# Optimization experiments

Hardware: AMD Instinct MI355X
Metric: run time of the kernel (lower is better)

Reference implementation:

```python
import jax, jax.numpy as jnp
import numpy as np

CHUNK = 64
NORM_EPS = 1e-5
DENOM_EPS = 1.0
B, S, HID, H = 4, 4096, 1024, 8
D = HID // H  # 128


def rmsnorm(x, w, eps=NORM_EPS):
    var = jnp.mean(x * x, axis=-1, keepdims=True)
    return x * jax.lax.rsqrt(var + eps) * w


def chunked_linear_attn(q, k, v):
    # q,k,v: [B,S,H,D]; causal linear attention o_s = q_s @ sum_{t<=s} k_t^T v_t
    b, s, h, d = q.shape
    n = s // CHUNK
    def to_chunks(x):
        return x.reshape(b, n, CHUNK, h, d).transpose(1, 0, 3, 2, 4)  # [N,B,H,C,D]
    qc, kc, vc = to_chunks(q), to_chunks(k), to_chunks(v)
    mask = jnp.tril(jnp.ones((CHUNK, CHUNK), dtype=q.dtype))
    def step(state, inp):
        qq, kk, vv = inp  # [B,H,C,D]
        inter = jnp.einsum('bhcd,bhde->bhce', qq, state)
        scores = jnp.einsum('bhcd,bhed->bhce', qq, kk) * mask  # causal intra-chunk
        intra = jnp.einsum('bhce,bhed->bhcd', scores, vv)
        state = state + jnp.einsum('bhcd,bhce->bhde', kk, vv)
        return state, inter + intra
    init = jnp.zeros((b, h, d, d), dtype=q.dtype)
    _, o = jax.lax.scan(step, init, (qc, kc, vc))  # [N,B,H,C,D]
    return o.transpose(1, 0, 3, 2, 4).reshape(b, s, h, d)


def setup_inputs() -> dict:
    key = jax.random.key(0)
    k0, k1, k2, k3, k4 = jax.random.split(key, 5)
    hidden_states = jax.random.normal(k0, (B, S, HID), dtype=jnp.float32)
    Wq = jax.random.normal(k1, (HID, HID), dtype=jnp.float32) * 0.02
    Wk = jax.random.normal(k2, (HID, HID), dtype=jnp.float32) * 0.02
    Wv = jax.random.normal(k3, (HID, HID), dtype=jnp.float32) * 0.02
    Wo = jax.random.normal(k4, (HID, HID), dtype=jnp.float32) * 0.02
    norm_w = jnp.ones((D,), dtype=jnp.float32)
    return {"hidden_states": hidden_states, "Wq": Wq, "Wk": Wk, "Wv": Wv, "Wo": Wo, "norm_w": norm_w}


def reference(hidden_states, Wq, Wk, Wv, Wo, norm_w):
    b, s, _ = hidden_states.shape
    q = jnp.einsum('bsd,ed->bse', hidden_states, Wq).reshape(b, s, H, D)
    k = jnp.einsum('bsd,ed->bse', hidden_states, Wk).reshape(b, s, H, D)
    v = jnp.einsum('bsd,ed->bse', hidden_states, Wv).reshape(b, s, H, D)
    # feature_map='identity', norm_q/norm_k=False
    o = chunked_linear_attn(q, k, v)  # [B,S,H,D]
    z = jnp.cumsum(k, axis=1)
    denom = jnp.maximum(jnp.abs(jnp.sum(q * z, axis=-1)), DENOM_EPS)[..., None]
    o = o / denom
    o = rmsnorm(o, norm_w)
    o = o.reshape(b, s, H * D)
    return jnp.einsum('bse,de->bsd', o, Wo)
```

## Files before the change

kernel.cpp:

```cpp
#include <hip/hip_runtime.h>
#include <stdint.h>

typedef __bf16 bf16x8 __attribute__((ext_vector_type(8)));
typedef float  f32x4  __attribute__((ext_vector_type(4)));

static __device__ __forceinline__ void gload16(const void* g, void* l) {
  __builtin_amdgcn_global_load_lds((__attribute__((address_space(1))) void*)g,
                                   (__attribute__((address_space(3))) void*)l,
                                   16, 0, 0);
}

static __device__ __forceinline__ f32x4 mfma16(bf16x8 a, bf16x8 b, f32x4 c) {
  return __builtin_amdgcn_mfma_f32_16x16x32_bf16(a, b, c, 0, 0, 0);
}

#define MEMFENCE asm volatile("" ::: "memory")

__global__ __launch_bounds__(256) void cast8_k(const float* __restrict__ in,
                                               __bf16* __restrict__ out) {
  const size_t i = ((size_t)blockIdx.x * 256 + threadIdx.x) * 8;
  const float4 v0 = *(const float4*)(in + i);
  const float4 v1 = *(const float4*)(in + i + 4);
  bf16x8 o;
  o[0] = (__bf16)v0.x; o[1] = (__bf16)v0.y; o[2] = (__bf16)v0.z; o[3] = (__bf16)v0.w;
  o[4] = (__bf16)v1.x; o[5] = (__bf16)v1.y; o[6] = (__bf16)v1.z; o[7] = (__bf16)v1.w;
  *(bf16x8*)(out + i) = o;
}

__global__ __launch_bounds__(256) void castw_k(const float* __restrict__ w0, const float* __restrict__ w1,
                                               const float* __restrict__ w2, const float* __restrict__ w3,
                                               __bf16* __restrict__ o0, __bf16* __restrict__ o1,
                                               __bf16* __restrict__ o2, __bf16* __restrict__ o3) {
  const float* in; __bf16* out;
  switch (blockIdx.y) {
    case 0: in = w0; out = o0; break;
    case 1: in = w1; out = o1; break;
    case 2: in = w2; out = o2; break;
    default: in = w3; out = o3; break;
  }
  const size_t i = ((size_t)blockIdx.x * 256 + threadIdx.x) * 8;
  const float4 v0 = *(const float4*)(in + i);
  const float4 v1 = *(const float4*)(in + i + 4);
  bf16x8 o;
  o[0] = (__bf16)v0.x; o[1] = (__bf16)v0.y; o[2] = (__bf16)v0.z; o[3] = (__bf16)v0.w;
  o[4] = (__bf16)v1.x; o[5] = (__bf16)v1.y; o[6] = (__bf16)v1.z; o[7] = (__bf16)v1.w;
  *(bf16x8*)(out + i) = o;
}

static __device__ __forceinline__ void kloop256(
    const __bf16* __restrict__ A, const __bf16* __restrict__ W,
    int m0, int n0, __bf16* sh, int tid, f32x4 acc[8][4]) {
  const int l = tid & 63;
  const int wv = tid >> 6;
  const int wm = wv >> 2, wn = wv & 3;
  const int lo = l & 15, kq = l >> 4;

  auto SA = [&](int kt, int h) {
#pragma unroll
    for (int j = 0; j < 2; ++j) {
      const int p = j * 512 + tid;
      const int r = p >> 3, sl = p & 7;
      const int grow = m0 + h * 64 + (r & 63) + (r >> 6) * 128;
      gload16(A + (size_t)grow * 1024 + (kt << 6) + ((sl ^ (r & 7)) << 3),
              sh + (kt & 1) * 32768 + h * 8192 + p * 8);
    }
  };
  auto SB = [&](int kt, int h) {
#pragma unroll
    for (int j = 0; j < 2; ++j) {
      const int p = j * 512 + tid;
      const int r = p >> 3, sl = p & 7;
      const int grow = n0 + h * 32 + (r & 31) + (r >> 5) * 64;
      gload16(W + (size_t)grow * 1024 + (kt << 6) + ((sl ^ (r & 7)) << 3),
              sh + (kt & 1) * 32768 + 16384 + h * 8192 + p * 8);
    }
  };
  auto LDA = [&](int cur, int mh, int mi, int ks) -> bf16x8 {
    const int r = wm * 64 + mi * 16 + lo;
    return *(const bf16x8*)&sh[cur * 32768 + mh * 8192 + r * 64 + (((ks * 4 + kq) ^ (r & 7)) << 3)];
  };
  auto LDB = [&](int cur, int nh, int ni, int ks) -> bf16x8 {
    const int r = wn * 32 + ni * 16 + lo;
    return *(const bf16x8*)&sh[cur * 32768 + 16384 + nh * 8192 + r * 64 + (((ks * 4 + kq) ^ (r & 7)) << 3)];
  };

  SA(0, 0); SB(0, 0); SB(0, 1); SA(0, 1);
  SA(1, 0); SB(1, 1); SA(1, 1);
  MEMFENCE;
  asm volatile("s_waitcnt vmcnt(6)" ::: "memory");
  __builtin_amdgcn_s_barrier();

  bf16x8 a[4][2], b[2][2], b2[2][2];
#pragma unroll 2
  for (int t = 0; t < 16; ++t) {
    const int cur = t & 1;
#pragma unroll
    for (int mi = 0; mi < 4; ++mi)
#pragma unroll
      for (int ks = 0; ks < 2; ++ks) a[mi][ks] = LDA(cur, 0, mi, ks);
#pragma unroll
    for (int ni = 0; ni < 2; ++ni)
#pragma unroll
      for (int ks = 0; ks < 2; ++ks) b[ni][ks] = LDB(cur, 0, ni, ks);
    if (t + 1 < 16) SB(t + 1, 0);
    MEMFENCE;
    __builtin_amdgcn_s_barrier();
    asm volatile("s_waitcnt lgkmcnt(0)" ::: "memory");
    __builtin_amdgcn_sched_barrier(0);
    __builtin_amdgcn_s_setprio(1);
#pragma unroll
    for (int mi = 0; mi < 4; ++mi)
#pragma unroll
      for (int ni = 0; ni < 2; ++ni)
#pragma unroll
        for (int ks = 0; ks < 2; ++ks)
          acc[mi][ni] = mfma16(a[mi][ks], b[ni][ks], acc[mi][ni]);
    __builtin_amdgcn_s_setprio(0);
    MEMFENCE;
    __builtin_amdgcn_s_barrier();
#pragma unroll
    for (int ni = 0; ni < 2; ++ni)
#pragma unroll
      for (int ks = 0; ks < 2; ++ks) b2[ni][ks] = LDB(cur, 1, ni, ks);
    if (t + 2 < 16) SA(t + 2, 0);
    MEMFENCE;
    __builtin_amdgcn_s_barrier();
    asm volatile("s_waitcnt lgkmcnt(0)" ::: "memory");
    __builtin_amdgcn_sched_barrier(0);
    __builtin_amdgcn_s_setprio(1);
#pragma unroll
    for (int mi = 0; mi < 4; ++mi)
#pragma unroll
      for (int ni = 0; ni < 2; ++ni)
#pragma unroll
        for (int ks = 0; ks < 2; ++ks)
          acc[mi][2 + ni] = mfma16(a[mi][ks], b2[ni][ks], acc[mi][2 + ni]);
    __builtin_amdgcn_s_setprio(0);
    MEMFENCE;
    __builtin_amdgcn_s_barrier();
#pragma unroll
    for (int mi = 0; mi < 4; ++mi)
#pragma unroll
      for (int ks = 0; ks < 2; ++ks) a[mi][ks] = LDA(cur, 1, mi, ks);
    if (t + 2 < 16) SB(t + 2, 1);
    MEMFENCE;
    __builtin_amdgcn_s_barrier();
    asm volatile("s_waitcnt lgkmcnt(0)" ::: "memory");
    __builtin_amdgcn_sched_barrier(0);
    __builtin_amdgcn_s_setprio(1);
#pragma unroll
    for (int mi = 0; mi < 4; ++mi)
#pragma unroll
      for (int ni = 0; ni < 2; ++ni)
#pragma unroll
        for (int ks = 0; ks < 2; ++ks)
          acc[4 + mi][2 + ni] = mfma16(a[mi][ks], b2[ni][ks], acc[4 + mi][2 + ni]);
    __builtin_amdgcn_s_setprio(0);
    MEMFENCE;
    __builtin_amdgcn_s_barrier();
#pragma unroll
    for (int ni = 0; ni < 2; ++ni)
#pragma unroll
      for (int ks = 0; ks < 2; ++ks) b[ni][ks] = LDB(cur, 0, ni, ks);
    if (t + 2 < 16) SA(t + 2, 1);
    MEMFENCE;
    __builtin_amdgcn_s_barrier();
    asm volatile("s_waitcnt lgkmcnt(0)" ::: "memory");
    __builtin_amdgcn_sched_barrier(0);
    __builtin_amdgcn_s_setprio(1);
#pragma unroll
    for (int mi = 0; mi < 4; ++mi)
#pragma unroll
      for (int ni = 0; ni < 2; ++ni)
#pragma unroll
        for (int ks = 0; ks < 2; ++ks)
          acc[4 + mi][ni] = mfma16(a[mi][ks], b[ni][ks], acc[4 + mi][ni]);
    __builtin_amdgcn_s_setprio(0);
    if (t < 14) asm volatile("s_waitcnt vmcnt(6)" ::: "memory");
    else        asm volatile("s_waitcnt vmcnt(0)" ::: "memory");
    MEMFENCE;
    __builtin_amdgcn_s_barrier();
  }
}

__global__ __launch_bounds__(512, 2)
void gemm_qkv8_k(const __bf16* __restrict__ A,
                 const __bf16* __restrict__ Bq, const __bf16* __restrict__ Bk, const __bf16* __restrict__ Bv,
                 __bf16* __restrict__ Qo, __bf16* __restrict__ Ko,
                 __bf16* __restrict__ Kt, __bf16* __restrict__ Vt) {
  extern __shared__ __bf16 sh[];
  const int tid = threadIdx.x;
  const int flat = blockIdx.x;
  const int sf = (flat & 7) * 96 + (flat >> 3);
  const int z = sf >> 8;
  const int rem = sf & 255;
  const int m0 = (rem >> 2) * 256;
  const int n0 = (rem & 3) * 256;
  const __bf16* W = (z == 0) ? Bq : (z == 1) ? Bk : Bv;

  f32x4 acc[8][4] = {};
  kloop256(A, W, m0, n0, sh, tid, acc);

  const int l = tid & 63, wv = tid >> 6, wm = wv >> 2, wn = wv & 3;
  const int lo = l & 15, kq = l >> 4;

  if (z <= 1) {
    __bf16* R = z ? Ko : Qo;
#pragma unroll
    for (int nh = 0; nh < 2; ++nh) {
      if ((wn >> 1) == nh) {
#pragma unroll
        for (int mi = 0; mi < 8; ++mi)
#pragma unroll
          for (int ni = 0; ni < 4; ++ni)
#pragma unroll
            for (int rr = 0; rr < 4; ++rr)
              sh[wm * 17408 + (mi * 16 + kq * 4 + rr) * 136 + (wn & 1) * 64 + ni * 16 + lo]
                  = (__bf16)acc[mi][ni][rr];
      }
      __syncthreads();
#pragma unroll
      for (int it = 0; it < 8; ++it) {
        const int idx = it * 512 + tid;
        const int rg = idx >> 11, mrow = (idx >> 4) & 127, sl = idx & 15;
        *(bf16x8*)(R + (size_t)(m0 + rg * 128 + mrow) * 1024 + n0 + nh * 128 + sl * 8)
            = *(const bf16x8*)&sh[rg * 17408 + mrow * 136 + sl * 8];
      }
      __syncthreads();
    }
  }
  if (z >= 1) {
    __bf16* T = (z == 1) ? Kt : Vt;
    const int bb = m0 >> 12, s0v = m0 & 4095, h0 = n0 >> 7;
#pragma unroll
    for (int nh = 0; nh < 2; ++nh) {
      if ((wn >> 1) == nh) {
#pragma unroll
        for (int mi = 0; mi < 8; ++mi)
#pragma unroll
          for (int ni = 0; ni < 4; ++ni)
#pragma unroll
            for (int rr = 0; rr < 4; ++rr)
              sh[wm * 17408 + ((wn & 1) * 64 + ni * 16 + lo) * 136 + mi * 16 + kq * 4 + rr]
                  = (__bf16)acc[mi][ni][rr];
      }
      __syncthreads();
      const int hh = h0 + nh;
#pragma unroll
      for (int it = 0; it < 8; ++it) {
        const int idx = it * 512 + tid;
        const int rg = idx >> 11, dr = (idx >> 4) & 127, sl = idx & 15;
        *(bf16x8*)(T + ((size_t)((bb * 8 + hh) * 128 + dr)) * 4096 + s0v + rg * 128 + sl * 8)
            = *(const bf16x8*)&sh[rg * 17408 + dr * 136 + sl * 8];
      }
      __syncthreads();
    }
  }
}

__global__ __launch_bounds__(512, 2)
void gemm_out8_k(const __bf16* __restrict__ A, const __bf16* __restrict__ W,
                 float* __restrict__ Co) {
  extern __shared__ __bf16 sh[];
  const int tid = threadIdx.x;
  const int flat = blockIdx.x;
  const int sf = (flat & 7) * 32 + (flat >> 3);
  const int m0 = (sf >> 2) * 256;
  const int n0 = (sf & 3) * 256;

  f32x4 acc[8][4] = {};
  kloop256(A, W, m0, n0, sh, tid, acc);

  const int l = tid & 63, wv = tid >> 6, wm = wv >> 2, wn = wv & 3;
  const int lo = l & 15, kq = l >> 4;
#pragma unroll
  for (int mi = 0; mi < 8; ++mi)
#pragma unroll
    for (int ni = 0; ni < 4; ++ni)
#pragma unroll
      for (int rr = 0; rr < 4; ++rr)
        Co[(size_t)(m0 + wm * 128 + mi * 16 + kq * 4 + rr) * 1024 + n0 + wn * 64 + ni * 16 + lo]
            = acc[mi][ni][rr];
}

__global__ __launch_bounds__(128)
void z1_k(const __bf16* __restrict__ K, float* __restrict__ zc) {
  const int c = blockIdx.x, bh = blockIdx.y;
  const int bb = bh >> 3, hh = bh & 7;
  const int d = threadIdx.x;
  float a = 0.0f;
  for (int t = 0; t < 64; ++t)
    a += (float)K[((size_t)(bb * 4096 + c * 64 + t)) * 1024 + hh * 128 + d];
  zc[(size_t)(bh * 64 + c) * 128 + d] = a;
}

__global__ __launch_bounds__(128)
void z2_k(float* __restrict__ zc) {
  const int bh = blockIdx.x;
  const int d = threadIdx.x;
  float run = 0.0f;
  for (int cc = 0; cc < 64; ++cc) {
    float* p = zc + (size_t)(bh * 64 + cc) * 128 + d;
    const float old = *p;
    *p = run;
    run += old;
  }
}

__global__ __launch_bounds__(256)
void passA_k(const __bf16* __restrict__ Kt, const __bf16* __restrict__ Vt,
             __bf16* __restrict__ Sc) {
  const int c = blockIdx.x, bh = blockIdx.y;
  const int tid = threadIdx.x, l = tid & 63, w = tid >> 6;
  const int wr = (w >> 1) * 64, wc = (w & 1) * 64;
  const int lr = l & 15, lk = (l >> 4) * 8;
  f32x4 acc[4][4] = {};
#pragma unroll
  for (int kk = 0; kk < 2; ++kk) {
    const int t = c * 64 + kk * 32 + lk;
    bf16x8 av[4], bk[4];
#pragma unroll
    for (int mt = 0; mt < 4; ++mt)
      av[mt] = *(const bf16x8*)(Vt + ((size_t)(bh * 128 + wr + mt * 16 + lr)) * 4096 + t);
#pragma unroll
    for (int nt = 0; nt < 4; ++nt)
      bk[nt] = *(const bf16x8*)(Kt + ((size_t)(bh * 128 + wc + nt * 16 + lr)) * 4096 + t);
#pragma unroll
    for (int mt = 0; mt < 4; ++mt)
#pragma unroll
      for (int nt = 0; nt < 4; ++nt)
        acc[mt][nt] = mfma16(av[mt], bk[nt], acc[mt][nt]);
  }
  const size_t sbase = ((size_t)(bh * 64 + c)) << 14;
#pragma unroll
  for (int mt = 0; mt < 4; ++mt)
#pragma unroll
    for (int r = 0; r < 4; ++r) {
      const int e = wr + mt * 16 + (l >> 4) * 4 + r;
#pragma unroll
      for (int nt = 0; nt < 4; ++nt) {
        const int d = wc + nt * 16 + lr;
        Sc[sbase + (size_t)e * 128 + d] = (__bf16)acc[mt][nt][r];
      }
    }
}

__global__ __launch_bounds__(256)
void passB_k(__bf16* __restrict__ Sc) {
  const int bh = blockIdx.y;
  const int idx = blockIdx.x * 256 + threadIdx.x;
  float run = 0.0f;
  for (int cc = 0; cc < 64; ++cc) {
    __bf16* p = Sc + (((size_t)(bh * 64 + cc)) << 14) + idx;
    const float old = (float)*p;
    *p = (__bf16)run;
    run += old;
  }
}

__global__ __launch_bounds__(256)
void passC_k(const __bf16* __restrict__ Q, const __bf16* __restrict__ K,
             const __bf16* __restrict__ Vt, const __bf16* __restrict__ Sp,
             const float* __restrict__ zp, const float* __restrict__ nw,
             __bf16* __restrict__ O) {
  alignas(16) __shared__ __bf16 ScL[64 * 72];
  alignas(16) __shared__ float OL[64 * 132];
  alignas(16) __shared__ float zPL[128];
  alignas(16) __shared__ float nwL[128];
  alignas(16) __shared__ float dnL[64];
  const int c = blockIdx.x, bh = blockIdx.y;
  const int bb = bh >> 3, hh = bh & 7;
  const int tid = threadIdx.x, l = tid & 63, wv = tid >> 6;
  const int lr = l & 15, lk = (l >> 4) * 8;
  if (tid < 128) zPL[tid] = zp[(size_t)(bh * 64 + c) * 128 + tid];
  else nwL[tid - 128] = nw[tid - 128];

  const size_t qbase = ((size_t)(bb * 4096 + c * 64)) * 1024 + hh * 128;
  const size_t sbase = ((size_t)(bh * 64 + c)) << 14;

  f32x4 accO[4][2] = {};
  f32x4 accS[4] = {};
#pragma unroll
  for (int kk = 0; kk < 4; ++kk) {
    const int dof = kk * 32 + lk;
    bf16x8 aQ[4], bS[2], bK;
#pragma unroll
    for (int mt = 0; mt < 4; ++mt)
      aQ[mt] = *(const bf16x8*)(Q + qbase + (size_t)(mt * 16 + lr) * 1024 + dof);
#pragma unroll
    for (int nt = 0; nt < 2; ++nt)
      bS[nt] = *(const bf16x8*)(Sp + sbase + (size_t)(wv * 32 + nt * 16 + lr) * 128 + dof);
    bK = *(const bf16x8*)(K + qbase + (size_t)(wv * 16 + lr) * 1024 + dof);
#pragma unroll
    for (int mt = 0; mt < 4; ++mt) {
      accS[mt] = mfma16(aQ[mt], bK, accS[mt]);
#pragma unroll
      for (int nt = 0; nt < 2; ++nt)
        accO[mt][nt] = mfma16(aQ[mt], bS[nt], accO[mt][nt]);
    }
  }
#pragma unroll
  for (int mt = 0; mt < 4; ++mt)
#pragma unroll
    for (int r = 0; r < 4; ++r) {
      const int srow = mt * 16 + (l >> 4) * 4 + r;
      const int tcol = wv * 16 + lr;
      ScL[srow * 72 + tcol] = (__bf16)((tcol <= srow) ? accS[mt][r] : 0.0f);
    }
  __syncthreads();
#pragma unroll
  for (int kk2 = 0; kk2 < 2; ++kk2) {
    const int tof = kk2 * 32 + lk;
    bf16x8 aS[4], bV[2];
#pragma unroll
    for (int mt = 0; mt < 4; ++mt) aS[mt] = *(const bf16x8*)&ScL[(mt * 16 + lr) * 72 + tof];
#pragma unroll
    for (int nt = 0; nt < 2; ++nt)
      bV[nt] = *(const bf16x8*)(Vt + ((size_t)(bh * 128 + wv * 32 + nt * 16 + lr)) * 4096 + c * 64 + tof);
#pragma unroll
    for (int mt = 0; mt < 4; ++mt)
#pragma unroll
      for (int nt = 0; nt < 2; ++nt)
        accO[mt][nt] = mfma16(aS[mt], bV[nt], accO[mt][nt]);
  }
  if (tid < 64) {
    float rs = 0.0f;
    for (int t = 0; t < 64; ++t) rs += (float)ScL[tid * 72 + t];
    float qz = 0.0f;
    const __bf16* qrow = Q + qbase + (size_t)tid * 1024;
#pragma unroll
    for (int j = 0; j < 16; ++j) {
      const bf16x8 q8 = *(const bf16x8*)(qrow + j * 8);
#pragma unroll
      for (int i = 0; i < 8; ++i) qz += (float)q8[i] * zPL[j * 8 + i];
    }
    dnL[tid] = fmaxf(fabsf(qz + rs), 1.0f);
  }
  __syncthreads();
#pragma unroll
  for (int mt = 0; mt < 4; ++mt)
#pragma unroll
    for (int r = 0; r < 4; ++r) {
      const int row = mt * 16 + (l >> 4) * 4 + r;
#pragma unroll
      for (int nt = 0; nt < 2; ++nt) {
        const int col = wv * 32 + nt * 16 + lr;
        OL[row * 132 + col] = accO[mt][nt][r] / dnL[row];
      }
    }
  __syncthreads();
  const int s = tid >> 2, e0 = (tid & 3) * 32;
  float ss = 0.0f;
  for (int i = 0; i < 32; ++i) { const float v = OL[s * 132 + e0 + i]; ss += v * v; }
  ss += __shfl_xor(ss, 1);
  ss += __shfl_xor(ss, 2);
  const float scale = rsqrtf(ss * (1.0f / 128.0f) + 1e-5f);
  __bf16* orow = O + qbase + (size_t)s * 1024 + e0;
#pragma unroll
  for (int i8 = 0; i8 < 4; ++i8) {
    bf16x8 ov;
#pragma unroll
    for (int j = 0; j < 8; ++j) {
      const int e = e0 + i8 * 8 + j;
      ov[j] = (__bf16)(OL[s * 132 + e] * scale * nwL[e]);
    }
    *(bf16x8*)(orow + i8 * 8) = ov;
  }
}

extern "C" void kernel_launch(void* const* d_in, const int* in_sizes, int n_in,
                              void* d_out, int out_size, void* d_ws, size_t ws_size,
                              hipStream_t stream) {
  (void)in_sizes; (void)n_in; (void)out_size; (void)ws_size;
  const float* hid = (const float*)d_in[0];
  const float* Wq  = (const float*)d_in[1];
  const float* Wk  = (const float*)d_in[2];
  const float* Wv  = (const float*)d_in[3];
  const float* Wo  = (const float*)d_in[4];
  const float* nw  = (const float*)d_in[5];

  char* ws = (char*)d_ws;
  size_t off = 0;
  auto nxt = [&](size_t bytes) -> char* {
    char* p = ws + off;
    off += (bytes + 255) & ~(size_t)255;
    return p;
  };
  __bf16* hA  = (__bf16*)nxt(33554432);
  __bf16* wqB = (__bf16*)nxt(2097152);
  __bf16* wkB = (__bf16*)nxt(2097152);
  __bf16* wvB = (__bf16*)nxt(2097152);
  __bf16* woB = (__bf16*)nxt(2097152);
  __bf16* Qb  = (__bf16*)nxt(33554432);
  __bf16* Kb  = (__bf16*)nxt(33554432);
  __bf16* Ktb = (__bf16*)nxt(33554432);
  __bf16* Vtb = (__bf16*)nxt(33554432);
  __bf16* Scb = (__bf16*)nxt(67108864);
  float*  zcb = (float*)nxt(1048576);
  __bf16* Ob  = hA;

  cast8_k<<<8192, 256, 0, stream>>>(hid, hA);
  castw_k<<<dim3(512, 4), 256, 0, stream>>>(Wq, Wk, Wv, Wo, wqB, wkB, wvB, woB);
  gemm_qkv8_k<<<768, 512, 131072, stream>>>(hA, wqB, wkB, wvB, Qb, Kb, Ktb, Vtb);
  z1_k<<<dim3(64, 32), 128, 0, stream>>>(Kb, zcb);
  passA_k<<<dim3(64, 32), 256, 0, stream>>>(Ktb, Vtb, Scb);
  passB_k<<<dim3(64, 32), 256, 0, stream>>>(Scb);
  z2_k<<<32, 128, 0, stream>>>(zcb);
  passC_k<<<dim3(64, 32), 256, 0, stream>>>(Qb, Kb, Vtb, Scb, zcb, nw, Ob);
  gemm_out8_k<<<256, 512, 131072, stream>>>(Ob, woB, (float*)d_out);
}
```

Measured before the change: 385.7 us.

## Fuse K chunk sums into passA, drop GEMM barriers, parallelize denominator

Computes the per-chunk column sums of K inside passA from the K tiles it already loads, reducing across lanes with shuffles, and deletes the separate z1 kernel launch and its strided re-read of K. It also removes the barrier that sat between LDS fragment loads and the MFMA block in each GEMM sub-step. The passC denominator work is split across all 256 threads with shuffle reductions instead of only 64. Dropping the barriers relies on the remaining barriers to keep LDS buffer reuse safe.

Result: faster. 368.1 us (-4.6%).

```diff
diff --git a/kernel.cpp b/kernel.cpp
--- a/kernel.cpp
+++ b/kernel.cpp
@@ -104,7 +104,6 @@
       for (int ks = 0; ks < 2; ++ks) b[ni][ks] = LDB(cur, 0, ni, ks);
     if (t + 1 < 16) SB(t + 1, 0);
     MEMFENCE;
-    __builtin_amdgcn_s_barrier();
     asm volatile("s_waitcnt lgkmcnt(0)" ::: "memory");
     __builtin_amdgcn_sched_barrier(0);
     __builtin_amdgcn_s_setprio(1);
@@ -124,7 +123,6 @@
       for (int ks = 0; ks < 2; ++ks) b2[ni][ks] = LDB(cur, 1, ni, ks);
     if (t + 2 < 16) SA(t + 2, 0);
     MEMFENCE;
-    __builtin_amdgcn_s_barrier();
     asm volatile("s_waitcnt lgkmcnt(0)" ::: "memory");
     __builtin_amdgcn_sched_barrier(0);
     __builtin_amdgcn_s_setprio(1);
@@ -144,7 +142,6 @@
       for (int ks = 0; ks < 2; ++ks) a[mi][ks] = LDA(cur, 1, mi, ks);
     if (t + 2 < 16) SB(t + 2, 1);
     MEMFENCE;
-    __builtin_amdgcn_s_barrier();
     asm volatile("s_waitcnt lgkmcnt(0)" ::: "memory");
     __builtin_amdgcn_sched_barrier(0);
     __builtin_amdgcn_s_setprio(1);
@@ -164,7 +161,6 @@
       for (int ks = 0; ks < 2; ++ks) b[ni][ks] = LDB(cur, 0, ni, ks);
     if (t + 2 < 16) SA(t + 2, 1);
     MEMFENCE;
-    __builtin_amdgcn_s_barrier();
     asm volatile("s_waitcnt lgkmcnt(0)" ::: "memory");
     __builtin_amdgcn_sched_barrier(0);
     __builtin_amdgcn_s_setprio(1);
@@ -284,17 +280,6 @@
 }
 
 __global__ __launch_bounds__(128)
-void z1_k(const __bf16* __restrict__ K, float* __restrict__ zc) {
-  const int c = blockIdx.x, bh = blockIdx.y;
-  const int bb = bh >> 3, hh = bh & 7;
-  const int d = threadIdx.x;
-  float a = 0.0f;
-  for (int t = 0; t < 64; ++t)
-    a += (float)K[((size_t)(bb * 4096 + c * 64 + t)) * 1024 + hh * 128 + d];
-  zc[(size_t)(bh * 64 + c) * 128 + d] = a;
-}
-
-__global__ __launch_bounds__(128)
 void z2_k(float* __restrict__ zc) {
   const int bh = blockIdx.x;
   const int d = threadIdx.x;
@@ -309,12 +294,13 @@
 
 __global__ __launch_bounds__(256)
 void passA_k(const __bf16* __restrict__ Kt, const __bf16* __restrict__ Vt,
-             __bf16* __restrict__ Sc) {
+             __bf16* __restrict__ Sc, float* __restrict__ zc) {
   const int c = blockIdx.x, bh = blockIdx.y;
   const int tid = threadIdx.x, l = tid & 63, w = tid >> 6;
   const int wr = (w >> 1) * 64, wc = (w & 1) * 64;
   const int lr = l & 15, lk = (l >> 4) * 8;
   f32x4 acc[4][4] = {};
+  float zac[4] = {0.0f, 0.0f, 0.0f, 0.0f};
 #pragma unroll
   for (int kk = 0; kk < 2; ++kk) {
     const int t = c * 64 + kk * 32 + lk;
@@ -323,13 +309,26 @@
     for (int mt = 0; mt < 4; ++mt)
       av[mt] = *(const bf16x8*)(Vt + ((size_t)(bh * 128 + wr + mt * 16 + lr)) * 4096 + t);
 #pragma unroll
-    for (int nt = 0; nt < 4; ++nt)
+    for (int nt = 0; nt < 4; ++nt) {
       bk[nt] = *(const bf16x8*)(Kt + ((size_t)(bh * 128 + wc + nt * 16 + lr)) * 4096 + t);
+#pragma unroll
+      for (int e = 0; e < 8; ++e) zac[nt] += (float)bk[nt][e];
+    }
 #pragma unroll
     for (int mt = 0; mt < 4; ++mt)
 #pragma unroll
       for (int nt = 0; nt < 4; ++nt)
         acc[mt][nt] = mfma16(av[mt], bk[nt], acc[mt][nt]);
+  }
+#pragma unroll
+  for (int nt = 0; nt < 4; ++nt) {
+    zac[nt] += __shfl_xor(zac[nt], 16);
+    zac[nt] += __shfl_xor(zac[nt], 32);
+  }
+  if (w < 2 && l < 16) {
+#pragma unroll
+    for (int nt = 0; nt < 4; ++nt)
+      zc[(size_t)(bh * 64 + c) * 128 + wc + nt * 16 + lr] = zac[nt];
   }
   const size_t sbase = ((size_t)(bh * 64 + c)) << 14;
 #pragma unroll
@@ -423,18 +422,23 @@
       for (int nt = 0; nt < 2; ++nt)
         accO[mt][nt] = mfma16(aS[mt], bV[nt], accO[mt][nt]);
   }
-  if (tid < 64) {
+  {
+    const int s = tid >> 2, grp = tid & 3;
     float rs = 0.0f;
-    for (int t = 0; t < 64; ++t) rs += (float)ScL[tid * 72 + t];
+#pragma unroll
+    for (int t = 0; t < 16; ++t) rs += (float)ScL[s * 72 + grp * 16 + t];
     float qz = 0.0f;
-    const __bf16* qrow = Q + qbase + (size_t)tid * 1024;
-#pragma unroll
-    for (int j = 0; j < 16; ++j) {
+    const __bf16* qrow = Q + qbase + (size_t)s * 1024 + grp * 32;
+#pragma unroll
+    for (int j = 0; j < 4; ++j) {
       const bf16x8 q8 = *(const bf16x8*)(qrow + j * 8);
 #pragma unroll
-      for (int i = 0; i < 8; ++i) qz += (float)q8[i] * zPL[j * 8 + i];
-    }
-    dnL[tid] = fmaxf(fabsf(qz + rs), 1.0f);
+      for (int i = 0; i < 8; ++i) qz += (float)q8[i] * zPL[grp * 32 + j * 8 + i];
+    }
+    float v = rs + qz;
+    v += __shfl_xor(v, 1);
+    v += __shfl_xor(v, 2);
+    if (grp == 0) dnL[s] = fmaxf(fabsf(v), 1.0f);
   }
   __syncthreads();
 #pragma unroll
@@ -502,8 +506,7 @@
   cast8_k<<<8192, 256, 0, stream>>>(hid, hA);
   castw_k<<<dim3(512, 4), 256, 0, stream>>>(Wq, Wk, Wv, Wo, wqB, wkB, wvB, woB);
   gemm_qkv8_k<<<768, 512, 131072, stream>>>(hA, wqB, wkB, wvB, Qb, Kb, Ktb, Vtb);
-  z1_k<<<dim3(64, 32), 128, 0, stream>>>(Kb, zcb);
-  passA_k<<<dim3(64, 32), 256, 0, stream>>>(Ktb, Vtb, Scb);
+  passA_k<<<dim3(64, 32), 256, 0, stream>>>(Ktb, Vtb, Scb, zcb);
   passB_k<<<dim3(64, 32), 256, 0, stream>>>(Scb);
   z2_k<<<32, 128, 0, stream>>>(zcb);
   passC_k<<<dim3(64, 32), 256, 0, stream>>>(Qb, Kb, Vtb, Scb, zcb, nw, Ob);
```
